# Optimization experiments

Hardware: AMD Instinct MI355X
Metric: run time of the kernel (lower is better)

The kernel has to match this reference:

```python
import jax, jax.numpy as jnp
import numpy as np

BATCH = 8192
DIM = 256
TEMP = 0.001
EPS = 1e-12  # torch F.normalize eps


def setup_inputs() -> dict:
    key = jax.random.key(0)
    k1, k2 = jax.random.split(key)
    proj_1 = jax.random.normal(k1, (BATCH, DIM), dtype=jnp.float32)
    proj_2 = jax.random.normal(k2, (BATCH, DIM), dtype=jnp.float32)
    return {"proj_1": proj_1, "proj_2": proj_2}


def _l2_normalize(x):
    norm = jnp.maximum(jnp.linalg.norm(x, axis=1, keepdims=True), EPS)
    return x / norm


def reference(proj_1, proj_2):
    # L2-normalize rows (SimCLR z_i, z_j)
    z_i = _l2_normalize(proj_1)  # [B, D]
    z_j = _l2_normalize(proj_2)  # [B, D]
    # cosine similarity of unit vectors == dot product -> single matmul
    sim = jnp.einsum("id,jd->ij", z_i, z_j)  # [B, B]
    positives = jnp.diagonal(sim)  # [B]
    n = positives / TEMP
    all_losses = -n + jax.scipy.special.logsumexp(sim / TEMP, axis=1)
    loss = jnp.sum(all_losses) / BATCH
    return (loss, jnp.sum(positives))
```

## Files before the change

### kernel.cpp

```cpp
#include <hip/hip_runtime.h>
#include <hip/hip_fp8.h>
#include <stdint.h>
#include <stddef.h>

#define BATCH 8192
#define DIM   256

#define LN2F 0.6931471805599453f
#define SCALE_ZJ 16.0f
#define SCALE_ZI 90.16844005556021f

typedef int   v8i    __attribute__((ext_vector_type(8)));
typedef float f32x16 __attribute__((ext_vector_type(16)));

static __device__ __forceinline__ uint8_t f2fp8(float f) {
  __hip_fp8_e4m3 q(f);
  return *reinterpret_cast<uint8_t*>(&q);
}

static __device__ __forceinline__ void stage8(const uint8_t* __restrict__ src,
                                              uint8_t* dst, int tid) {
  const int lane = tid & 63;
  const int w    = tid >> 6;
#pragma unroll
  for (int c = 0; c < 2; ++c) {
    const int L  = (c * 4 + w) * 1024 + lane * 16;
    const int Ls = L ^ (((L >> 8) & 7) << 4);
    __builtin_amdgcn_global_load_lds(
        (const __attribute__((address_space(1))) void*)(src + Ls),
        (__attribute__((address_space(3))) void*)(dst + (c * 4 + w) * 1024),
        16, 0, 0);
  }
}

__global__ __launch_bounds__(256) void prep_kernel(
    const float* __restrict__ p1, const float* __restrict__ p2,
    uint8_t* __restrict__ Zi8, uint8_t* __restrict__ Zj8,
    float* __restrict__ pos) {
  const int lane = threadIdx.x & 63;
  const int w    = threadIdx.x >> 6;
  const int row  = blockIdx.x * 4 + w;

  const float4 x1 = ((const float4*)p1)[row * 64 + lane];
  const float4 x2 = ((const float4*)p2)[row * 64 + lane];
  float ss1 = x1.x * x1.x + x1.y * x1.y + x1.z * x1.z + x1.w * x1.w;
  float ss2 = x2.x * x2.x + x2.y * x2.y + x2.z * x2.z + x2.w * x2.w;
  float d   = x1.x * x2.x + x1.y * x2.y + x1.z * x2.z + x1.w * x2.w;
#pragma unroll
  for (int m = 1; m < 64; m <<= 1) {
    ss1 += __shfl_xor(ss1, m);
    ss2 += __shfl_xor(ss2, m);
    d   += __shfl_xor(d, m);
  }
  const float n1 = fmaxf(sqrtf(ss1), 1e-12f);
  const float n2 = fmaxf(sqrtf(ss2), 1e-12f);
  if (lane == 0) pos[row] = d / (n1 * n2);

  const float sI = SCALE_ZI / n1;
  const float sJ = SCALE_ZJ / n2;
  uchar4 u1, u2;
  u1.x = f2fp8(x1.x * sI); u1.y = f2fp8(x1.y * sI);
  u1.z = f2fp8(x1.z * sI); u1.w = f2fp8(x1.w * sI);
  u2.x = f2fp8(x2.x * sJ); u2.y = f2fp8(x2.y * sJ);
  u2.z = f2fp8(x2.z * sJ); u2.w = f2fp8(x2.w * sJ);
  ((uchar4*)Zi8)[row * 64 + lane] = u1;
  ((uchar4*)Zj8)[row * 64 + lane] = u2;
}

static __device__ __forceinline__ void lse_update(const f32x16& acc,
                                                  float& m, float& l) {
  float t0 = fmaxf(fmaxf(acc[0],  acc[1]),  acc[2]);
  float t1 = fmaxf(fmaxf(acc[3],  acc[4]),  acc[5]);
  float t2 = fmaxf(fmaxf(acc[6],  acc[7]),  acc[8]);
  float t3 = fmaxf(fmaxf(acc[9],  acc[10]), acc[11]);
  t0 = fmaxf(fmaxf(t0, t1), fmaxf(fmaxf(acc[12], acc[13]), acc[14]));
  t2 = fmaxf(fmaxf(t2, t3), acc[15]);
  const float mn = fmaxf(m, fmaxf(t0, t2));
  float s0 = 0.f, s1 = 0.f;
#pragma unroll
  for (int r = 0; r < 16; r += 2) {
    s0 += __builtin_amdgcn_exp2f(acc[r + 0] - mn);
    s1 += __builtin_amdgcn_exp2f(acc[r + 1] - mn);
  }
  l = l * __builtin_amdgcn_exp2f(m - mn) + (s0 + s1);
  m = mn;
}

__global__ __launch_bounds__(256, 3) void lse_kernel(
    const uint8_t* __restrict__ Zi8, const uint8_t* __restrict__ Zj8,
    float* __restrict__ plse) {
  const int bid   = blockIdx.x;
  const int chunk = bid & 31;
  const int rb    = bid >> 5;
  const int tid   = threadIdx.x;
  const int lane  = tid & 63;
  const int w     = tid >> 6;
  const int r32   = lane & 31;
  const int h     = lane >> 5;
  const int iBase = rb * 256 + w * 64;

  __shared__ __align__(16) uint8_t lds[4][8192];

  v8i b0[4], b1[4];
  const uint8_t* zb = Zi8 + (size_t)(iBase + r32) * 256 + h * 32;
#pragma unroll
  for (int q = 0; q < 4; ++q) {
    union { int4 i4[2]; v8i v; } u0, u1;
    u0.i4[0] = *(const int4*)(zb + q * 64);
    u0.i4[1] = *(const int4*)(zb + q * 64 + 16);
    u1.i4[0] = *(const int4*)(zb + 32 * 256 + q * 64);
    u1.i4[1] = *(const int4*)(zb + 32 * 256 + q * 64 + 16);
    b0[q] = u0.v; b1[q] = u1.v;
  }
#pragma unroll
  for (int q = 0; q < 4; ++q) { asm("" : "+v"(b0[q])); asm("" : "+v"(b1[q])); }

  float m0 = -1e30f, l0 = 0.f, m1 = -1e30f, l1 = 0.f;

  const uint8_t* src = Zj8 + (size_t)chunk * (256 * 256);
  const int xm = (r32 & 7) << 4;

  stage8(src, &lds[0][0], tid);
  stage8(src + 8192, &lds[1][0], tid);

  for (int s = 0; s < 4; ++s) {
    __syncthreads();
    if (s < 3) {
      stage8(src + (size_t)(2 * s + 2) * 8192, &lds[(2 * s + 2) & 3][0], tid);
      stage8(src + (size_t)(2 * s + 3) * 8192, &lds[(2 * s + 3) & 3][0], tid);
    }
#pragma unroll
    for (int sub = 0; sub < 2; ++sub) {
      const uint8_t* buf = &lds[(2 * s + sub) & 3][0] + r32 * 256;
      f32x16 acc0 = {}, acc1 = {};
      __builtin_amdgcn_s_setprio(1);
#pragma unroll
      for (int q = 0; q < 4; ++q) {
        union { int4 i4[2]; v8i v; } ua;
        const int off0 = ((q * 64) | (h * 32)) ^ xm;
        const int off1 = ((q * 64 + 16) | (h * 32)) ^ xm;
        ua.i4[0] = *(const int4*)(buf + off0);
        ua.i4[1] = *(const int4*)(buf + off1);
        acc0 = __builtin_amdgcn_mfma_scale_f32_32x32x64_f8f6f4(
            ua.v, b0[q], acc0, 0, 0, 0, 0x7F7F7F7F, 0, 0x7F7F7F7F);
        acc1 = __builtin_amdgcn_mfma_scale_f32_32x32x64_f8f6f4(
            ua.v, b1[q], acc1, 0, 0, 0, 0x7F7F7F7F, 0, 0x7F7F7F7F);
      }
      __builtin_amdgcn_s_setprio(0);
      lse_update(acc0, m0, l0);
      lse_update(acc1, m1, l1);
    }
  }

#pragma unroll
  for (int p = 0; p < 2; ++p) {
    float m = p ? m1 : m0;
    float l = p ? l1 : l0;
    const float mo = __shfl_xor(m, 32);
    const float lo = __shfl_xor(l, 32);
    const float mn = fmaxf(m, mo);
    l = l * __builtin_amdgcn_exp2f(m - mn) + lo * __builtin_amdgcn_exp2f(mo - mn);
    if (h == 0) {
      const int i = iBase + p * 32 + r32;
      plse[(size_t)i * 32 + chunk] = mn + __builtin_amdgcn_logf(l);
    }
  }
}

__global__ __launch_bounds__(256) void finalize1_kernel(
    const float* __restrict__ plse, const float* __restrict__ pos,
    float2* __restrict__ bpart) {
  const int tid = threadIdx.x;
  const int row = blockIdx.x * 256 + tid;
  float v[32];
#pragma unroll
  for (int c = 0; c < 8; ++c) {
    const float4 q = ((const float4*)(plse + (size_t)row * 32))[c];
    v[c * 4 + 0] = q.x; v[c * 4 + 1] = q.y; v[c * 4 + 2] = q.z; v[c * 4 + 3] = q.w;
  }
  float M = v[0];
#pragma unroll
  for (int c = 1; c < 32; ++c) M = fmaxf(M, v[c]);
  float S = 0.0f;
#pragma unroll
  for (int c = 0; c < 32; ++c) S += __builtin_amdgcn_exp2f(v[c] - M);
  const float lse = LN2F * (M + __builtin_amdgcn_logf(S));
  const float pv  = pos[row];
  float lsum = lse - 1000.0f * pv;
  float psum = pv;
#pragma unroll
  for (int msk = 1; msk < 64; msk <<= 1) {
    lsum += __shfl_xor(lsum, msk);
    psum += __shfl_xor(psum, msk);
  }
  __shared__ float sl[4], sp[4];
  const int w = tid >> 6, lane = tid & 63;
  if (lane == 0) { sl[w] = lsum; sp[w] = psum; }
  __syncthreads();
  if (tid == 0) {
    bpart[blockIdx.x] = make_float2(sl[0] + sl[1] + sl[2] + sl[3],
                                    sp[0] + sp[1] + sp[2] + sp[3]);
  }
}

__global__ __launch_bounds__(64) void finalize2_kernel(
    const float2* __restrict__ bpart, float* __restrict__ out) {
  const int tid = threadIdx.x;
  float L = 0.0f, P = 0.0f;
  if (tid < 32) { const float2 v = bpart[tid]; L = v.x; P = v.y; }
#pragma unroll
  for (int msk = 1; msk < 64; msk <<= 1) {
    L += __shfl_xor(L, msk);
    P += __shfl_xor(P, msk);
  }
  if (tid == 0) {
    out[0] = L / (float)BATCH;
    out[1] = P;
  }
}

extern "C" void kernel_launch(void* const* d_in, const int* in_sizes, int n_in,
                              void* d_out, int out_size, void* d_ws, size_t ws_size,
                              hipStream_t stream) {
  const float* p1 = (const float*)d_in[0];
  const float* p2 = (const float*)d_in[1];
  float* out = (float*)d_out;
  uint8_t* ws = (uint8_t*)d_ws;

  uint8_t* Zi8    = ws;
  uint8_t* Zj8    = ws + (size_t)2 * 1024 * 1024;
  float* pos      = (float*)(ws + (size_t)4 * 1024 * 1024);
  float2* bpart   = (float2*)(ws + (size_t)4 * 1024 * 1024 + 32 * 1024);
  float* plse     = (float*)(ws + (size_t)4 * 1024 * 1024 + 64 * 1024);

  prep_kernel<<<dim3(2048), dim3(256), 0, stream>>>(p1, p2, Zi8, Zj8, pos);
  lse_kernel<<<dim3(1024), dim3(256), 0, stream>>>(Zi8, Zj8, plse);
  finalize1_kernel<<<dim3(32), dim3(256), 0, stream>>>(plse, pos, bpart);
  finalize2_kernel<<<dim3(1), dim3(64), 0, stream>>>(bpart, out);
}
```

Baseline: 40.40 us.

## Pre-tile fp8 operands into MFMA fragment layout and fuse final reduction

The prep kernel now writes the fp8 Zi/Zj matrices in a tiled layout that matches the MFMA operand fragments. This lets the LSE kernel stage LDS with plain contiguous copies and read fragments without XOR swizzle arithmetic. The two finalize kernels merge into one that uses a last-block atomic counter, at the cost of an extra memset launch. Occupancy bounds also rise from 3 to 4 blocks per SM, which risks register pressure and LDS bank conflicts now that the swizzle is gone.

```diff
diff --git a/kernel.cpp b/kernel.cpp
--- a/kernel.cpp
+++ b/kernel.cpp
@@ -13,6 +13,7 @@
 typedef int   v8i    __attribute__((ext_vector_type(8)));
 typedef float f32x16 __attribute__((ext_vector_type(16)));
 
+
 static __device__ __forceinline__ uint8_t f2fp8(float f) {
   __hip_fp8_e4m3 q(f);
   return *reinterpret_cast<uint8_t*>(&q);
@@ -20,15 +21,12 @@
 
 static __device__ __forceinline__ void stage8(const uint8_t* __restrict__ src,
                                               uint8_t* dst, int tid) {
-  const int lane = tid & 63;
-  const int w    = tid >> 6;
-#pragma unroll
-  for (int c = 0; c < 2; ++c) {
-    const int L  = (c * 4 + w) * 1024 + lane * 16;
-    const int Ls = L ^ (((L >> 8) & 7) << 4);
+#pragma unroll
+  for (int it = 0; it < 2; ++it) {
+    const int off = it * 4096 + tid * 16;
     __builtin_amdgcn_global_load_lds(
-        (const __attribute__((address_space(1))) void*)(src + Ls),
-        (__attribute__((address_space(3))) void*)(dst + (c * 4 + w) * 1024),
+        (const __attribute__((address_space(1))) void*)(src + off),
+        (__attribute__((address_space(3))) void*)(dst + off),
         16, 0, 0);
   }
 }
@@ -63,8 +61,12 @@
   u1.z = f2fp8(x1.z * sI); u1.w = f2fp8(x1.w * sI);
   u2.x = f2fp8(x2.x * sJ); u2.y = f2fp8(x2.y * sJ);
   u2.z = f2fp8(x2.z * sJ); u2.w = f2fp8(x2.w * sJ);
-  ((uchar4*)Zi8)[row * 64 + lane] = u1;
-  ((uchar4*)Zj8)[row * 64 + lane] = u2;
+
+  const size_t tb = (size_t)(row >> 5) * 8192;
+  const int off = (lane >> 4) * 2048 + ((lane >> 2) & 1) * 1024 +
+                  (((lane >> 3) & 1) * 32 + (row & 31)) * 16 + (lane & 3) * 4;
+  *(uchar4*)(Zi8 + tb + off) = u1;
+  *(uchar4*)(Zj8 + tb + off) = u2;
 }
 
 static __device__ __forceinline__ void lse_update(const f32x16& acc,
@@ -86,7 +88,7 @@
   m = mn;
 }
 
-__global__ __launch_bounds__(256, 3) void lse_kernel(
+__global__ __launch_bounds__(256, 4) void lse_kernel(
     const uint8_t* __restrict__ Zi8, const uint8_t* __restrict__ Zj8,
     float* __restrict__ plse) {
   const int bid   = blockIdx.x;
@@ -102,14 +104,14 @@
   __shared__ __align__(16) uint8_t lds[4][8192];
 
   v8i b0[4], b1[4];
-  const uint8_t* zb = Zi8 + (size_t)(iBase + r32) * 256 + h * 32;
+  const uint8_t* zb = Zi8 + (size_t)(rb * 8 + w * 2) * 8192 + lane * 16;
 #pragma unroll
   for (int q = 0; q < 4; ++q) {
     union { int4 i4[2]; v8i v; } u0, u1;
-    u0.i4[0] = *(const int4*)(zb + q * 64);
-    u0.i4[1] = *(const int4*)(zb + q * 64 + 16);
-    u1.i4[0] = *(const int4*)(zb + 32 * 256 + q * 64);
-    u1.i4[1] = *(const int4*)(zb + 32 * 256 + q * 64 + 16);
+    u0.i4[0] = *(const int4*)(zb + q * 2048);
+    u0.i4[1] = *(const int4*)(zb + q * 2048 + 1024);
+    u1.i4[0] = *(const int4*)(zb + 8192 + q * 2048);
+    u1.i4[1] = *(const int4*)(zb + 8192 + q * 2048 + 1024);
     b0[q] = u0.v; b1[q] = u1.v;
   }
 #pragma unroll
@@ -117,8 +119,7 @@
 
   float m0 = -1e30f, l0 = 0.f, m1 = -1e30f, l1 = 0.f;
 
-  const uint8_t* src = Zj8 + (size_t)chunk * (256 * 256);
-  const int xm = (r32 & 7) << 4;
+  const uint8_t* src = Zj8 + (size_t)chunk * (8 * 8192);
 
   stage8(src, &lds[0][0], tid);
   stage8(src + 8192, &lds[1][0], tid);
@@ -131,16 +132,14 @@
     }
 #pragma unroll
     for (int sub = 0; sub < 2; ++sub) {
-      const uint8_t* buf = &lds[(2 * s + sub) & 3][0] + r32 * 256;
+      const uint8_t* buf = &lds[(2 * s + sub) & 3][0] + lane * 16;
       f32x16 acc0 = {}, acc1 = {};
       __builtin_amdgcn_s_setprio(1);
 #pragma unroll
       for (int q = 0; q < 4; ++q) {
         union { int4 i4[2]; v8i v; } ua;
-        const int off0 = ((q * 64) | (h * 32)) ^ xm;
-        const int off1 = ((q * 64 + 16) | (h * 32)) ^ xm;
-        ua.i4[0] = *(const int4*)(buf + off0);
-        ua.i4[1] = *(const int4*)(buf + off1);
+        ua.i4[0] = *(const int4*)(buf + q * 2048);
+        ua.i4[1] = *(const int4*)(buf + q * 2048 + 1024);
         acc0 = __builtin_amdgcn_mfma_scale_f32_32x32x64_f8f6f4(
             ua.v, b0[q], acc0, 0, 0, 0, 0x7F7F7F7F, 0, 0x7F7F7F7F);
         acc1 = __builtin_amdgcn_mfma_scale_f32_32x32x64_f8f6f4(
@@ -167,9 +166,10 @@
   }
 }
 
-__global__ __launch_bounds__(256) void finalize1_kernel(
+__global__ __launch_bounds__(256) void finalize_kernel(
     const float* __restrict__ plse, const float* __restrict__ pos,
-    float2* __restrict__ bpart) {
+    float2* __restrict__ bpart, unsigned int* __restrict__ counter,
+    float* __restrict__ out) {
   const int tid = threadIdx.x;
   const int row = blockIdx.x * 256 + tid;
   float v[32];
@@ -198,24 +198,25 @@
   if (lane == 0) { sl[w] = lsum; sp[w] = psum; }
   __syncthreads();
   if (tid == 0) {
-    bpart[blockIdx.x] = make_float2(sl[0] + sl[1] + sl[2] + sl[3],
-                                    sp[0] + sp[1] + sp[2] + sp[3]);
-  }
-}
-
-__global__ __launch_bounds__(64) void finalize2_kernel(
-    const float2* __restrict__ bpart, float* __restrict__ out) {
-  const int tid = threadIdx.x;
-  float L = 0.0f, P = 0.0f;
-  if (tid < 32) { const float2 v = bpart[tid]; L = v.x; P = v.y; }
-#pragma unroll
-  for (int msk = 1; msk < 64; msk <<= 1) {
-    L += __shfl_xor(L, msk);
-    P += __shfl_xor(P, msk);
-  }
-  if (tid == 0) {
-    out[0] = L / (float)BATCH;
-    out[1] = P;
+    union { float2 f; unsigned long long u; } pk;
+    pk.f = make_float2(sl[0] + sl[1] + sl[2] + sl[3],
+                       sp[0] + sp[1] + sp[2] + sp[3]);
+    __hip_atomic_store((unsigned long long*)&bpart[blockIdx.x], pk.u,
+                       __ATOMIC_RELEASE, __HIP_MEMORY_SCOPE_AGENT);
+    const unsigned int t = __hip_atomic_fetch_add(
+        counter, 1u, __ATOMIC_ACQ_REL, __HIP_MEMORY_SCOPE_AGENT);
+    if (t == 31u) {
+      float L = 0.f, P = 0.f;
+#pragma unroll
+      for (int i = 0; i < 32; ++i) {
+        union { float2 f; unsigned long long u; } q2;
+        q2.u = __hip_atomic_load((const unsigned long long*)&bpart[i],
+                                 __ATOMIC_ACQUIRE, __HIP_MEMORY_SCOPE_AGENT);
+        L += q2.f.x; P += q2.f.y;
+      }
+      out[0] = L / (float)BATCH;
+      out[1] = P;
+    }
   }
 }
 
@@ -227,14 +228,15 @@
   float* out = (float*)d_out;
   uint8_t* ws = (uint8_t*)d_ws;
 
-  uint8_t* Zi8    = ws;
-  uint8_t* Zj8    = ws + (size_t)2 * 1024 * 1024;
-  float* pos      = (float*)(ws + (size_t)4 * 1024 * 1024);
-  float2* bpart   = (float2*)(ws + (size_t)4 * 1024 * 1024 + 32 * 1024);
-  float* plse     = (float*)(ws + (size_t)4 * 1024 * 1024 + 64 * 1024);
-
+  uint8_t* Zi8          = ws;
+  uint8_t* Zj8          = ws + (size_t)2 * 1024 * 1024;
+  float* pos            = (float*)(ws + (size_t)4 * 1024 * 1024);
+  float2* bpart         = (float2*)(ws + (size_t)4 * 1024 * 1024 + 32 * 1024);
+  unsigned int* counter = (unsigned int*)(ws + (size_t)4 * 1024 * 1024 + 40 * 1024);
+  float* plse           = (float*)(ws + (size_t)4 * 1024 * 1024 + 64 * 1024);
+
+  hipMemsetAsync(counter, 0, sizeof(unsigned int), stream);
   prep_kernel<<<dim3(2048), dim3(256), 0, stream>>>(p1, p2, Zi8, Zj8, pos);
   lse_kernel<<<dim3(1024), dim3(256), 0, stream>>>(Zi8, Zj8, plse);
-  finalize1_kernel<<<dim3(32), dim3(256), 0, stream>>>(plse, pos, bpart);
-  finalize2_kernel<<<dim3(1), dim3(64), 0, stream>>>(bpart, out);
-}
+  finalize_kernel<<<dim3(32), dim3(256), 0, stream>>>(plse, pos, bpart, counter, out);
+}
```

Result: slower. 86.54 us (+114.2%).
